# Kernel tuning notes

Measured on AMD Instinct MI355X. Metric: run time of the kernel, lower is better.

The kernel has to match this reference:

```python
import jax, jax.numpy as jnp
import numpy as np
import math

N_STATE = 64
H_MODEL = 1024
D_CONV = 16
EXPAND = 2
D_INNER = EXPAND * H_MODEL            # 2048
HEADDIM = H_MODEL // 4                # 256
NHEADS = D_INNER // HEADDIM           # 8
NGROUPS = 1
CONV_DIM = D_INNER + 2 * NGROUPS * N_STATE           # 2176
D_IN_PROJ = 2 * D_INNER + 2 * NGROUPS * N_STATE + NHEADS
BATCH, SEQLEN = 4, 2048


def setup_inputs() -> dict:
    key = jax.random.key(0)
    ks = jax.random.split(key, 10)
    x = jax.random.normal(ks[0], (BATCH, SEQLEN, H_MODEL), jnp.float32)
    W_in = jax.random.normal(ks[1], (H_MODEL, D_IN_PROJ), jnp.float32) * (H_MODEL ** -0.5)
    conv_w = jax.random.normal(ks[2], (CONV_DIM, D_CONV), jnp.float32) * (D_CONV ** -0.5)
    conv_b = jnp.zeros((CONV_DIM,), jnp.float32)
    # inverse-softplus of dt0 in [1e-3, 1e-1] (mamba2 dt init)
    dt0 = jnp.exp(jax.random.uniform(ks[3], (NHEADS,), minval=math.log(1e-3), maxval=math.log(1e-1)))
    dt_bias = jnp.log(jnp.expm1(dt0))
    A_log = jnp.log(jax.random.uniform(ks[4], (NHEADS,), minval=1.0, maxval=16.0))
    D = jnp.ones((NHEADS,), jnp.float32)
    init_states = jax.random.normal(ks[5], (NHEADS, HEADDIM, N_STATE), jnp.float32) * 0.01
    norm_w = jnp.ones((D_INNER,), jnp.float32)
    W_out = jax.random.normal(ks[6], (D_INNER, H_MODEL), jnp.float32) * (D_INNER ** -0.5)
    W_nl = jax.random.normal(ks[7], (H_MODEL, H_MODEL), jnp.float32) * (H_MODEL ** -0.5)
    b_nl = jnp.zeros((H_MODEL,), jnp.float32)
    return dict(x=x, W_in=W_in, conv_w=conv_w, conv_b=conv_b, dt_bias=dt_bias,
                A_log=A_log, D=D, init_states=init_states, norm_w=norm_w,
                W_out=W_out, W_nl=W_nl, b_nl=b_nl)


def _mamba2(x, W_in, conv_w, conv_b, dt_bias, A_log, D, init_states, norm_w, W_out):
    b, l, _ = x.shape
    zxbcdt = x @ W_in                                  # (b, l, d_in_proj)
    z = zxbcdt[..., :D_INNER]
    xBC = zxbcdt[..., D_INNER:D_INNER + CONV_DIM]
    dt = jax.nn.softplus(zxbcdt[..., -NHEADS:] + dt_bias)   # (b, l, nheads)
    # depthwise causal conv1d (torch conv1d == cross-correlation)
    kernel = conv_w.T[:, None, :]                      # (K, 1, conv_dim)
    xBC = jax.lax.conv_general_dilated(
        xBC, kernel, window_strides=(1,), padding=[(D_CONV - 1, 0)],
        dimension_numbers=('NWC', 'WIO', 'NWC'), feature_group_count=CONV_DIM) + conv_b
    xBC = jax.nn.silu(xBC)
    xs = xBC[..., :D_INNER].reshape(b, l, NHEADS, HEADDIM)  # (b, l, h, p)
    Bm = xBC[..., D_INNER:D_INNER + N_STATE]                 # (b, l, n)
    Cm = xBC[..., D_INNER + N_STATE:]                        # (b, l, n)
    A = -jnp.exp(A_log)                                      # (nheads,) negative
    dA = jnp.exp(dt * A)                                     # (b, l, h)
    h0 = jnp.broadcast_to(init_states, (b, NHEADS, HEADDIM, N_STATE))

    def step(h, inp):
        dA_t, x_t, dt_t, B_t, C_t = inp
        dBx = jnp.einsum('bh,bhp,bn->bhpn', dt_t, x_t, B_t)
        h = h * dA_t[:, :, None, None] + dBx
        y_t = jnp.einsum('bhpn,bn->bhp', h, C_t)
        return h, y_t

    scan_in = (jnp.moveaxis(dA, 1, 0), jnp.moveaxis(xs, 1, 0), jnp.moveaxis(dt, 1, 0),
               jnp.moveaxis(Bm, 1, 0), jnp.moveaxis(Cm, 1, 0))
    _, ys = jax.lax.scan(step, h0, scan_in)
    y = jnp.moveaxis(ys, 0, 1) + D[None, None, :, None] * xs  # D skip connection
    y = y.reshape(b, l, D_INNER)
    # gated RMSNorm: rmsnorm(y * silu(z)) * norm_w, eps=1e-5
    y = y * jax.nn.silu(z)
    y = y * jax.lax.rsqrt(jnp.mean(y * y, axis=-1, keepdims=True) + 1e-5) * norm_w
    return y @ W_out


def reference(x, W_in, conv_w, conv_b, dt_bias, A_log, D, init_states, norm_w, W_out, W_nl, b_nl):
    y = _mamba2(x, W_in, conv_w, conv_b, dt_bias, A_log, D, init_states, norm_w, W_out)
    t = y / jnp.sqrt(1.0 + y * y)   # TanhApprox
    return t @ W_nl + b_nl + x      # Linear + residual
```

## Files before the change

kernel.cpp:

```cpp
#include <hip/hip_runtime.h>
#include <stdint.h>
#include <stddef.h>

#define BATCH   4
#define SEQLEN  2048
#define HM      1024
#define DINNER  2048
#define NH      8
#define HD      256
#define NS      64
#define CONVD   2176
#define DCONV   16
#define DPROJ   4232
#define ROWS    (BATCH*SEQLEN)
#define QC      256
#define NC      (SEQLEN/QC)
#define SC      64
#define TT      16

typedef __attribute__((ext_vector_type(8))) short short8;
typedef __attribute__((ext_vector_type(4))) short short4v;
typedef __attribute__((ext_vector_type(4))) float f32x4;

static constexpr size_t O_WOUT   = 0;
static constexpr size_t O_WNL    = 4194304;
static constexpr size_t O_DT     = 6291456;
static constexpr size_t O_LDA    = 6553600;
static constexpr size_t O_PG     = 6815744;
static constexpr size_t O_BT     = 6819840;
static constexpr size_t O_ZB     = 7868416;
static constexpr size_t O_XBCPRE = 41422848;
static constexpr size_t O_SG     = O_XBCPRE;
static constexpr size_t O_HG     = O_XBCPRE + 16777216;
static constexpr size_t O_TB     = O_XBCPRE;
static constexpr size_t O_XBC    = 77074432;
static constexpr size_t O_YN     = O_XBC;
static constexpr size_t O_XTR    = 112726016;
static constexpr size_t O_XBF    = O_XTR;
static constexpr size_t O_WIN    = O_XTR + 16777216;
static constexpr size_t O_WTAIL  = 146280448;

__device__ __forceinline__ short f2bf(float f) {
  union { float f; uint32_t u; } v; v.f = f;
  uint32_t r = v.u + 0x7fffu + ((v.u >> 16) & 1u);
  return (short)(r >> 16);
}

__device__ __forceinline__ float bf2f(short s) {
  union { float f; uint32_t u; } v;
  v.u = ((uint32_t)(uint16_t)s) << 16;
  return v.f;
}

__device__ __forceinline__ void gload_lds16(const void* g, void* l) {
  __builtin_amdgcn_global_load_lds(
      (const __attribute__((address_space(1))) uint32_t*)g,
      (__attribute__((address_space(3))) uint32_t*)l, 16, 0, 0);
}

__device__ __forceinline__ float sigmoidf_fast(float x) {
  return 1.f / (1.f + __expf(-x));
}

__device__ __forceinline__ short8 fragr(const char* base, int row, int kbyte) {
  return *(const short8*)(base + row * 128 + (kbyte ^ ((row & 7) << 4)));
}

__device__ __forceinline__ void transpose_tile(const float* __restrict__ W,
                                               short* __restrict__ Wt,
                                               int idx, int srcN, int validN,
                                               int Kdim, int nTilesN, int tid) {
  __shared__ short lds[64][72];
  int k0 = (idx / nTilesN) * 64;
  int n0 = (idx % nTilesN) * 64;
  int rr = tid >> 4;
  int cc = (tid & 15) * 4;
#pragma unroll
  for (int pass = 0; pass < 4; ++pass) {
    int k = pass * 16 + rr;
    int gn = n0 + cc;
    f32x4 v = (f32x4)0.f;
    if (gn < validN) v = *(const f32x4*)(W + (size_t)(k0 + k) * srcN + gn);
    uint32_t p0 = (uint32_t)(uint16_t)f2bf(v[0]) | ((uint32_t)(uint16_t)f2bf(v[1]) << 16);
    uint32_t p1 = (uint32_t)(uint16_t)f2bf(v[2]) | ((uint32_t)(uint16_t)f2bf(v[3]) << 16);
    *(uint32_t*)&lds[k][cc] = p0;
    *(uint32_t*)&lds[k][cc + 2] = p1;
  }
  __syncthreads();
  int n = tid >> 2;
  int ks = (tid & 3) * 16;
  short8 a, b;
#pragma unroll
  for (int j = 0; j < 8; ++j) a[j] = lds[ks + j][n];
#pragma unroll
  for (int j = 0; j < 8; ++j) b[j] = lds[ks + 8 + j][n];
  short* dst = Wt + (size_t)(n0 + n) * Kdim + k0 + ks;
  *(short8*)dst = a;
  *(short8*)(dst + 8) = b;
}

__global__ __launch_bounds__(256)
void prep_weights_kernel(const float* __restrict__ W_in, const float* __restrict__ W_out,
                         const float* __restrict__ W_nl,
                         short* __restrict__ winT, short* __restrict__ woutT,
                         short* __restrict__ wnlT, float* __restrict__ wtailT) {
  int bid = blockIdx.x, tid = threadIdx.x;
  if (bid < 1056) {
    transpose_tile(W_in, winT, bid, DPROJ, DPROJ, HM, 66, tid);
  } else if (bid < 1568) {
    transpose_tile(W_out, woutT, bid - 1056, HM, HM, DINNER, 16, tid);
  } else if (bid < 1824) {
    transpose_tile(W_nl, wnlT, bid - 1568, HM, HM, HM, 16, tid);
  } else {
    int i = (bid - 1824) * 256 + tid;
    int h = i >> 10, k = i & 1023;
    wtailT[i] = W_in[(size_t)k * DPROJ + (DPROJ - NH) + h];
  }
}

__global__ __launch_bounds__(256)
void cast_dt_kernel(const float* __restrict__ x, const float* __restrict__ wtailT,
                    const float* __restrict__ dt_bias, const float* __restrict__ A_log,
                    short* __restrict__ xbf, float* __restrict__ dtg,
                    float* __restrict__ ldA) {
  int row = blockIdx.x, tid = threadIdx.x;
  f32x4 xv = ((const f32x4*)(x + (size_t)row * HM))[tid];
  short4v o = { f2bf(xv[0]), f2bf(xv[1]), f2bf(xv[2]), f2bf(xv[3]) };
  ((short4v*)(xbf + (size_t)row * HM))[tid] = o;
  float p[NH];
#pragma unroll
  for (int h = 0; h < NH; ++h) {
    f32x4 w = ((const f32x4*)(wtailT + h * HM))[tid];
    p[h] = xv[0] * w[0] + xv[1] * w[1] + xv[2] * w[2] + xv[3] * w[3];
  }
#pragma unroll
  for (int h = 0; h < NH; ++h)
#pragma unroll
    for (int of = 32; of; of >>= 1) p[h] += __shfl_down(p[h], of);
  __shared__ float red[4][NH];
  int lane = tid & 63, w4 = tid >> 6;
  if (lane == 0)
#pragma unroll
    for (int h = 0; h < NH; ++h) red[w4][h] = p[h];
  __syncthreads();
  if (tid < NH) {
    float s = red[0][tid] + red[1][tid] + red[2][tid] + red[3][tid] + dt_bias[tid];
    float dtv = (s > 20.f) ? s : log1pf(expf(s));
    float A = -expf(A_log[tid]);
    dtg[row * NH + tid] = dtv;
    ldA[row * NH + tid] = dtv * A;
  }
}

__device__ __forceinline__ void prefix_aa(float av, float* aa, float* wsum,
                                          int tid) {
  float v = av;
  int lane = tid & 63;
#pragma unroll
  for (int o = 1; o < 64; o <<= 1) {
    float u = __shfl_up(v, o);
    if (lane >= o) v += u;
  }
  if (lane == 63) wsum[tid >> 6] = v;
  __syncthreads();
  float off = 0.f;
  int w4 = tid >> 6;
#pragma unroll
  for (int w = 0; w < 4; ++w)
    if (w < w4) off += wsum[w];
  aa[tid + 1] = v + off;
  if (tid == 0) aa[0] = 0.f;
  __syncthreads();
}

__global__ __launch_bounds__(512)
void gemm1_256(const short* __restrict__ A, const short* __restrict__ B,
               int K, int nTilesN,
               short* __restrict__ Cb, short* __restrict__ Cb2) {
  __shared__ alignas(16) char lds[49152];
  char* As = lds;
  char* Bs = lds + 32768;
  const int tid = threadIdx.x;
  int bid = blockIdx.x;
  {
    int nwg = gridDim.x;
    if ((nwg & 7) == 0) bid = (bid & 7) * (nwg >> 3) + (bid >> 3);
  }
  const int m0 = (bid / nTilesN) * 256;
  const int n0 = (bid % nTilesN) * 128;
  const int lane = tid & 63;
  const int wid = tid >> 6;
  const int wm = wid >> 1;
  const int wn = wid & 1;
  const int lrow = lane & 15, lk = lane >> 4;

  f32x4 acc[4][4];
#pragma unroll
  for (int i = 0; i < 4; ++i)
#pragma unroll
    for (int j = 0; j < 4; ++j) acc[i][j] = (f32x4)0.f;

  for (int k0 = 0; k0 < K; k0 += 64) {
#pragma unroll
    for (int r = 0; r < 4; ++r) {
      int p = r * 8192 + tid * 16;
      int row = p >> 7, c = p & 127;
      int sc = c ^ ((row & 7) << 4);
      gload_lds16((const char*)A + ((size_t)(m0 + row) * K + k0) * 2 + sc, As + p);
    }
#pragma unroll
    for (int r = 0; r < 2; ++r) {
      int p = r * 8192 + tid * 16;
      int row = p >> 7, c = p & 127;
      int sc = c ^ ((row & 7) << 4);
      gload_lds16((const char*)B + ((size_t)(n0 + row) * K + k0) * 2 + sc, Bs + p);
    }
    asm volatile("s_waitcnt vmcnt(0)" ::: "memory");
    __syncthreads();
#pragma unroll
    for (int ks = 0; ks < 2; ++ks) {
      short8 av[4], bv[4];
#pragma unroll
      for (int i = 0; i < 4; ++i) {
        av[i] = fragr(As, wm * 64 + i * 16 + lrow, ks * 64 + lk * 16);
        bv[i] = fragr(Bs, wn * 64 + i * 16 + lrow, ks * 64 + lk * 16);
      }
#pragma unroll
      for (int i = 0; i < 4; ++i)
#pragma unroll
        for (int j = 0; j < 4; ++j)
          acc[i][j] = __builtin_amdgcn_mfma_f32_16x16x32_bf16(av[i], bv[j], acc[i][j], 0, 0, 0);
    }
    __syncthreads();
  }

  const int row0 = m0 + wm * 64, col0 = n0 + wn * 64;
#pragma unroll
  for (int i = 0; i < 4; ++i)
#pragma unroll
    for (int j = 0; j < 4; ++j)
#pragma unroll
      for (int r = 0; r < 4; ++r) {
        int row = row0 + i * 16 + lk * 4 + r;
        int col = col0 + j * 16 + lrow;
        float v = acc[i][j][r];
        if (col < DINNER) Cb[(size_t)row * DINNER + col] = f2bf(v);
        else if (col < DINNER + CONVD) Cb2[(size_t)row * CONVD + (col - DINNER)] = f2bf(v);
      }
}

template <int EPI>
__global__ __launch_bounds__(512)
void gemm8p(const short* __restrict__ A, const short* __restrict__ B,
            int K, int nTilesN, int N_out,
            float* __restrict__ Cf, short* __restrict__ Cb,
            const float* __restrict__ bias, const float* __restrict__ resid) {
  __shared__ alignas(16) char lds[147456];
  const int tid = threadIdx.x;
  int bid = blockIdx.x;
  {
    int nwg = gridDim.x;
    if ((nwg & 7) == 0) bid = (bid & 7) * (nwg >> 3) + (bid >> 3);
  }
  const int m0 = (bid / nTilesN) * 256;
  const int n0 = (bid % nTilesN) * 128;
  const int lane = tid & 63;
  const int wid = tid >> 6;
  const int wm = wid >> 1;
  const int wn = wid & 1;
  const int lrow = lane & 15, lk = lane >> 4;
  const int nK = K >> 6;

#define LDSA(s) (lds + (s) * 49152)
#define LDSB(s) (lds + (s) * 49152 + 32768)

#define STAGE_A(s, kt, it) do {                                              \
    int p_ = (it) * 8192 + tid * 16;                                         \
    int row_ = p_ >> 7, c_ = p_ & 127;                                       \
    int sc_ = c_ ^ ((row_ & 7) << 4);                                        \
    gload_lds16((const char*)A + ((size_t)(m0 + row_) * K + (kt) * 64) * 2 + sc_, \
                LDSA(s) + p_);                                               \
  } while (0)
#define STAGE_B(s, kt, it) do {                                              \
    int p_ = (it) * 8192 + tid * 16;                                         \
    int row_ = p_ >> 7, c_ = p_ & 127;                                       \
    int sc_ = c_ ^ ((row_ & 7) << 4);                                        \
    gload_lds16((const char*)B + ((size_t)(n0 + row_) * K + (kt) * 64) * 2 + sc_, \
                LDSB(s) + p_);                                               \
  } while (0)

  f32x4 acc[4][4];
#pragma unroll
  for (int i = 0; i < 4; ++i)
#pragma unroll
    for (int j = 0; j < 4; ++j) acc[i][j] = (f32x4)0.f;

#pragma unroll
  for (int it = 0; it < 4; ++it) STAGE_A(0, 0, it);
#pragma unroll
  for (int it = 0; it < 2; ++it) STAGE_B(0, 0, it);
#pragma unroll
  for (int it = 0; it < 4; ++it) STAGE_A(1, 1, it);
#pragma unroll
  for (int it = 0; it < 2; ++it) STAGE_B(1, 1, it);
  asm volatile("s_waitcnt vmcnt(6)" ::: "memory");
  __builtin_amdgcn_s_barrier();

  for (int kt = 0; kt < nK; ++kt) {
    const int rs = kt % 3;
    const int ss = (kt + 2) % 3;
    const bool st = (kt + 2) < nK;
    const char* Ab = LDSA(rs);
    const char* Bb = LDSB(rs);
    short8 aF[4][2], bF[4][2];

#pragma unroll
    for (int ii = 0; ii < 4; ++ii)
#pragma unroll
      for (int ks = 0; ks < 2; ++ks)
        aF[ii][ks] = fragr(Ab, wm * 64 + ii * 16 + lrow, ks * 64 + lk * 16);
#pragma unroll
    for (int jj = 0; jj < 2; ++jj)
#pragma unroll
      for (int ks = 0; ks < 2; ++ks)
        bF[jj][ks] = fragr(Bb, wn * 64 + jj * 16 + lrow, ks * 64 + lk * 16);
    if (st) { STAGE_A(ss, kt + 2, 0); STAGE_A(ss, kt + 2, 1); STAGE_A(ss, kt + 2, 2); STAGE_A(ss, kt + 2, 3); }
    __builtin_amdgcn_s_barrier();
    asm volatile("s_waitcnt lgkmcnt(0)" ::: "memory");
    __builtin_amdgcn_s_setprio(1);
#pragma unroll
    for (int ii = 0; ii < 4; ++ii)
#pragma unroll
      for (int jj = 0; jj < 2; ++jj)
#pragma unroll
        for (int ks = 0; ks < 2; ++ks)
          acc[ii][jj] = __builtin_amdgcn_mfma_f32_16x16x32_bf16(aF[ii][ks], bF[jj][ks], acc[ii][jj], 0, 0, 0);
    __builtin_amdgcn_s_setprio(0);
    __builtin_amdgcn_s_barrier();

#pragma unroll
    for (int jj = 2; jj < 4; ++jj)
#pragma unroll
      for (int ks = 0; ks < 2; ++ks)
        bF[jj][ks] = fragr(Bb, wn * 64 + jj * 16 + lrow, ks * 64 + lk * 16);
    if (st) { STAGE_B(ss, kt + 2, 0); STAGE_B(ss, kt + 2, 1); }
    __builtin_amdgcn_s_barrier();
    asm volatile("s_waitcnt lgkmcnt(0)" ::: "memory");
    __builtin_amdgcn_s_setprio(1);
#pragma unroll
    for (int ii = 0; ii < 4; ++ii)
#pragma unroll
      for (int jj = 2; jj < 4; ++jj)
#pragma unroll
        for (int ks = 0; ks < 2; ++ks)
          acc[ii][jj] = __builtin_amdgcn_mfma_f32_16x16x32_bf16(aF[ii][ks], bF[jj][ks], acc[ii][jj], 0, 0, 0);
    __builtin_amdgcn_s_setprio(0);
    if (kt >= nK - 2) {
      asm volatile("s_waitcnt vmcnt(0)" ::: "memory");
    } else {
      asm volatile("s_waitcnt vmcnt(6)" ::: "memory");
    }
    __builtin_amdgcn_s_barrier();
  }

  const int row0 = m0 + wm * 64, col0 = n0 + wn * 64;
#pragma unroll
  for (int i = 0; i < 4; ++i)
#pragma unroll
    for (int j = 0; j < 4; ++j)
#pragma unroll
      for (int r = 0; r < 4; ++r) {
        int row = row0 + i * 16 + lk * 4 + r;
        int col = col0 + j * 16 + lrow;
        float v = acc[i][j][r];
        if (EPI == 1) {
          float t = v * rsqrtf(1.f + v * v);
          Cb[(size_t)row * N_out + col] = f2bf(t);
        } else if (EPI == 2) {
          Cf[(size_t)row * N_out + col] = v + bias[col] + resid[(size_t)row * N_out + col];
        }
      }
#undef LDSA
#undef LDSB
#undef STAGE_A
#undef STAGE_B
}

__global__ __launch_bounds__(256) void conv_silu_kernel(const short* __restrict__ xbcpre,
                                                        const float* __restrict__ cw,
                                                        const float* __restrict__ cbias,
                                                        short* __restrict__ bc,
                                                        short* __restrict__ xT,
                                                        short* __restrict__ bTg) {
  __shared__ short tld[64][130];
  int blk = blockIdx.x;
  int cg = blk % 17;
  int tg = (blk / 17) % 32;
  int b  = blk / (17 * 32);
  int lane = threadIdx.x & 63;
  int warp = threadIdx.x >> 6;
  int c0 = cg * 128 + lane * 2;
  int tbase = (tg * 4 + warp) * TT;

  const short* inp = xbcpre + (size_t)(b * SEQLEN) * CONVD + c0;
  uint32_t in[TT + DCONV - 1];
#pragma unroll
  for (int j = 0; j < TT + DCONV - 1; ++j) {
    int t = tbase + j - (DCONV - 1);
    in[j] = (t >= 0) ? *(const uint32_t*)(inp + (size_t)t * CONVD) : 0u;
  }
  float w0[DCONV], w1[DCONV];
  const float* wp = cw + (size_t)c0 * DCONV;
#pragma unroll
  for (int k = 0; k < DCONV; ++k) { w0[k] = wp[k]; w1[k] = wp[DCONV + k]; }
  float bb0 = cbias[c0], bb1 = cbias[c0 + 1];

  const bool isBC = (cg == 16);
  short* bcp = bc + (size_t)(b * SEQLEN) * 128 + (c0 - DINNER);
#pragma unroll
  for (int tt = 0; tt < TT; ++tt) {
    float a0 = bb0, a1 = bb1;
#pragma unroll
    for (int k = 0; k < DCONV; ++k) {
      uint32_t v = in[tt + k];
      a0 = fmaf(bf2f((short)(v & 0xffffu)), w0[k], a0);
      a1 = fmaf(bf2f((short)(v >> 16)), w1[k], a1);
    }
    a0 = a0 * sigmoidf_fast(a0);
    a1 = a1 * sigmoidf_fast(a1);
    uint32_t o = (uint32_t)(uint16_t)f2bf(a0) | ((uint32_t)(uint16_t)f2bf(a1) << 16);
    if (isBC) *(uint32_t*)(bcp + (size_t)(tbase + tt) * 128) = o;
    *(uint32_t*)&tld[warp * TT + tt][lane * 2] = o;
  }
  __syncthreads();
  int ch = threadIdx.x & 127;
  int seg = threadIdx.x >> 7;
  int gc = cg * 128 + ch;
  short* dst = nullptr;
  if (gc < DINNER) dst = xT + (size_t)gc * ROWS;
  else if (gc < DINNER + NS) dst = bTg + (size_t)(gc - DINNER) * ROWS;
  if (dst) {
    int tcol = b * SEQLEN + tg * 64 + seg * 32;
    short8 v[4];
#pragma unroll
    for (int q = 0; q < 4; ++q)
#pragma unroll
      for (int j = 0; j < 8; ++j) v[q][j] = tld[seg * 32 + q * 8 + j][ch];
    short8* dp = (short8*)(dst + tcol);
    dp[0] = v[0]; dp[1] = v[1]; dp[2] = v[2]; dp[3] = v[3];
  }
}

__global__ __launch_bounds__(256)
void scan_passA_mfma(const short* __restrict__ xT, const short* __restrict__ bTg,
                     const float* __restrict__ dtg, const float* __restrict__ ldA,
                     float* __restrict__ Sg, float* __restrict__ Pg) {
  __shared__ alignas(16) char Ax[16384];
  __shared__ alignas(16) char Bt[8192];
  __shared__ float aa[QC + 1];
  __shared__ float wdt[QC];
  __shared__ float wsum[4];
  int blk2 = blockIdx.x;
  int half = blk2 & 1, blk = blk2 >> 1;
  int c8 = blk & 7, bh = blk >> 3;
  int h = bh & 7, b = bh >> 3;
  int pbase = half * 128;
  int tid = threadIdx.x, wave = tid >> 6, lane = tid & 63;
  int lrow = lane & 15, lk = lane >> 4;
  int rowbase = b * SEQLEN + c8 * QC;
  prefix_aa(ldA[(rowbase + tid) * NH + h], aa, wsum, tid);
  float alast = aa[QC];
  if (tid == 0 && half == 0) Pg[blk] = __expf(alast);
  wdt[tid] = __expf(alast - aa[tid + 1]) * dtg[(rowbase + tid) * NH + h];

  f32x4 acc[2][4];
#pragma unroll
  for (int i = 0; i < 2; ++i)
#pragma unroll
    for (int j = 0; j < 4; ++j) acc[i][j] = (f32x4)0.f;

  for (int ks = 0; ks < 4; ++ks) {
    int s0 = ks * 64;
#pragma unroll
    for (int it = 0; it < 4; ++it) {
      int p = it * 4096 + tid * 16;
      int row = p >> 7, c = p & 127;
      int sc = c ^ ((row & 7) << 4);
      gload_lds16((const char*)(xT + (size_t)(h * HD + pbase + row) * ROWS + rowbase + s0) + sc, Ax + p);
    }
#pragma unroll
    for (int it = 0; it < 2; ++it) {
      int p = it * 4096 + tid * 16;
      int row = p >> 7, c = p & 127;
      int sc = c ^ ((row & 7) << 4);
      gload_lds16((const char*)(bTg + (size_t)row * ROWS + rowbase + s0) + sc, Bt + p);
    }
    asm volatile("s_waitcnt vmcnt(0)" ::: "memory");
    __syncthreads();
    {
      int row = wave * 32 + (lane & 31);
      int gb = (lane >> 5) * 4;
#pragma unroll
      for (int gi = 0; gi < 4; ++gi) {
        int g = gb + gi;
        int off = row * 128 + g * 16;
        int sb = s0 + (((g * 16) ^ ((row & 7) << 4)) >> 1);
        short8 v = *(short8*)(Ax + off);
        short8 o;
#pragma unroll
        for (int j = 0; j < 8; ++j) o[j] = f2bf(bf2f(v[j]) * wdt[sb + j]);
        *(short8*)(Ax + off) = o;
      }
    }
    __syncthreads();
#pragma unroll
    for (int kk = 0; kk < 2; ++kk) {
      short8 av[2], bv[4];
#pragma unroll
      for (int i = 0; i < 2; ++i)
        av[i] = fragr(Ax, wave * 32 + i * 16 + lrow, kk * 64 + lk * 16);
#pragma unroll
      for (int j = 0; j < 4; ++j)
        bv[j] = fragr(Bt, j * 16 + lrow, kk * 64 + lk * 16);
#pragma unroll
      for (int i = 0; i < 2; ++i)
#pragma unroll
        for (int j = 0; j < 4; ++j)
          acc[i][j] = __builtin_amdgcn_mfma_f32_16x16x32_bf16(av[i], bv[j], acc[i][j], 0, 0, 0);
    }
    __syncthreads();
  }
#pragma unroll
  for (int i = 0; i < 2; ++i)
#pragma unroll
    for (int j = 0; j < 4; ++j)
#pragma unroll
      for (int r = 0; r < 4; ++r) {
        int p = pbase + wave * 32 + i * 16 + lk * 4 + r;
        int n = j * 16 + lrow;
        Sg[((size_t)blk * 256 + p) * 64 + n] = acc[i][j][r];
      }
}

__global__ __launch_bounds__(256)
void scan_passB(const float* __restrict__ Sg, const float* __restrict__ Pg,
                const float* __restrict__ init, float* __restrict__ Hg) {
  int blk = blockIdx.x;
  int ptile = blk & 15, bh = blk >> 4;
  int h = bh & (NH - 1);
  int tid = threadIdx.x;
  size_t off = (size_t)ptile * 1024 + tid * 4;
  f32x4 hc = *(const f32x4*)(init + (size_t)h * HD * NS + off);
#pragma unroll 1
  for (int c = 0; c < NC; ++c) {
    *(f32x4*)(Hg + (size_t)(bh * NC + c) * 16384 + off) = hc;
    float P = Pg[bh * NC + c];
    f32x4 s = *(const f32x4*)(Sg + (size_t)(bh * NC + c) * 16384 + off);
    hc = P * hc + s;
  }
}

__global__ __launch_bounds__(256)
void scan_passC_mfma(const short* __restrict__ xT, const short* __restrict__ bTg,
                     const short* __restrict__ bc,
                     const float* __restrict__ dtg, const float* __restrict__ ldA,
                     const float* __restrict__ Hg, const float* __restrict__ Dp,
                     short* __restrict__ yfull) {
  __shared__ alignas(16) char Xb[16384];
  __shared__ alignas(16) char Hb[16384];
  __shared__ alignas(16) char Bn[8192];
  __shared__ alignas(16) char Cn[8192];
  __shared__ alignas(16) char Bt2[8192];
  __shared__ alignas(16) char Mm[8192];
  __shared__ float aa[QC + 1];
  __shared__ float dts[QC];
  __shared__ float wsum[4];
  int blk2 = blockIdx.x;
  int half = blk2 & 1, blk = blk2 >> 1;
  int c8 = blk & 7, bh = blk >> 3;
  int h = bh & 7, b = bh >> 3;
  int pbase = half * 128;
  int tid = threadIdx.x, wave = tid >> 6, lane = tid & 63;
  int lrow = lane & 15, lk = lane >> 4;
  int rowbase = b * SEQLEN + c8 * QC;
  prefix_aa(ldA[(rowbase + tid) * NH + h], aa, wsum, tid);
  dts[tid] = dtg[(rowbase + tid) * NH + h];
  __syncthreads();
  float Dh = Dp[h];

  f32x4 hcc[2][4];
  const float* hp = Hg + (size_t)blk * 16384;
#pragma unroll
  for (int i = 0; i < 2; ++i)
#pragma unroll
    for (int j = 0; j < 4; ++j)
#pragma unroll
      for (int r = 0; r < 4; ++r)
        hcc[i][j][r] = hp[(size_t)(pbase + wave * 32 + i * 16 + lk * 4 + r) * 64 + j * 16 + lrow];

  for (int sc = 0; sc < 4; ++sc) {
    int s0 = sc * SC;
#pragma unroll
    for (int i = 0; i < 2; ++i)
#pragma unroll
      for (int j = 0; j < 4; ++j)
#pragma unroll
        for (int r = 0; r < 4; ++r) {
          int pl = wave * 32 + i * 16 + lk * 4 + r;
          int n = j * 16 + lrow;
          *(short*)(Hb + pl * 128 + ((n * 2) ^ ((pl & 7) << 4))) = f2bf(hcc[i][j][r]);
        }
#pragma unroll
    for (int it = 0; it < 4; ++it) {
      int p = it * 4096 + tid * 16;
      int row = p >> 7, c = p & 127;
      int scz = c ^ ((row & 7) << 4);
      gload_lds16((const char*)(xT + (size_t)(h * HD + pbase + row) * ROWS + rowbase + s0) + scz, Xb + p);
    }
#pragma unroll
    for (int it = 0; it < 2; ++it) {
      int p = it * 4096 + tid * 16;
      int row = p >> 7, c = p & 127;
      int scz = c ^ ((row & 7) << 4);
      gload_lds16((const char*)(bc + (size_t)(rowbase + s0 + row) * 128) + scz, Bn + p);
      gload_lds16((const char*)(bc + (size_t)(rowbase + s0 + row) * 128 + NS) + scz, Cn + p);
      gload_lds16((const char*)(bTg + (size_t)row * ROWS + rowbase + s0) + scz, Bt2 + p);
    }
    asm volatile("s_waitcnt vmcnt(0)" ::: "memory");
    __syncthreads();

    f32x4 gcc[4];
#pragma unroll
    for (int j = 0; j < 4; ++j) gcc[j] = (f32x4)0.f;
#pragma unroll
    for (int kk = 0; kk < 2; ++kk) {
      short8 avc = fragr(Cn, wave * 16 + lrow, kk * 64 + lk * 16);
#pragma unroll
      for (int j = 0; j < 4; ++j) {
        short8 bvb = fragr(Bn, j * 16 + lrow, kk * 64 + lk * 16);
        gcc[j] = __builtin_amdgcn_mfma_f32_16x16x32_bf16(avc, bvb, gcc[j], 0, 0, 0);
      }
    }
#pragma unroll
    for (int j = 0; j < 4; ++j)
#pragma unroll
      for (int r = 0; r < 4; ++r) {
        int t = wave * 16 + lk * 4 + r;
        int s = j * 16 + lrow;
        float val = (s <= t) ? gcc[j][r] * __expf(aa[s0 + t + 1] - aa[s0 + s + 1]) * dts[s0 + s]
                             : 0.f;
        *(short*)(Mm + t * 128 + ((s * 2) ^ ((t & 7) << 4))) = f2bf(val);
      }
#pragma unroll
    for (int pass = 0; pass < 2; ++pass) {
      int t = wave * 16 + (lane >> 3) + pass * 8;
      int g = lane & 7;
      int off = t * 128 + g * 16;
      float fac = __expf(aa[s0 + t + 1] - aa[s0]);
      short8 v = *(short8*)(Cn + off);
      short8 o;
#pragma unroll
      for (int j = 0; j < 8; ++j) o[j] = f2bf(bf2f(v[j]) * fac);
      *(short8*)(Cn + off) = o;
    }
    __syncthreads();

    f32x4 ycc[4][2];
#pragma unroll
    for (int i = 0; i < 4; ++i)
#pragma unroll
      for (int j = 0; j < 2; ++j) ycc[i][j] = (f32x4)0.f;
#pragma unroll
    for (int kk = 0; kk < 2; ++kk) {
      short8 av[4], bv[2];
#pragma unroll
      for (int i = 0; i < 4; ++i)
        av[i] = fragr(Mm, i * 16 + lrow, kk * 64 + lk * 16);
#pragma unroll
      for (int j = 0; j < 2; ++j)
        bv[j] = fragr(Xb, wave * 32 + j * 16 + lrow, kk * 64 + lk * 16);
#pragma unroll
      for (int i = 0; i < 4; ++i)
#pragma unroll
        for (int j = 0; j < 2; ++j)
          ycc[i][j] = __builtin_amdgcn_mfma_f32_16x16x32_bf16(av[i], bv[j], ycc[i][j], 0, 0, 0);
    }
#pragma unroll
    for (int kk = 0; kk < 2; ++kk) {
      short8 av[4], bv[2];
#pragma unroll
      for (int i = 0; i < 4; ++i)
        av[i] = fragr(Cn, i * 16 + lrow, kk * 64 + lk * 16);
#pragma unroll
      for (int j = 0; j < 2; ++j)
        bv[j] = fragr(Hb, wave * 32 + j * 16 + lrow, kk * 64 + lk * 16);
#pragma unroll
      for (int i = 0; i < 4; ++i)
#pragma unroll
        for (int j = 0; j < 2; ++j)
          ycc[i][j] = __builtin_amdgcn_mfma_f32_16x16x32_bf16(av[i], bv[j], ycc[i][j], 0, 0, 0);
    }
#pragma unroll
    for (int i = 0; i < 4; ++i)
#pragma unroll
      for (int j = 0; j < 2; ++j)
#pragma unroll
        for (int r = 0; r < 4; ++r) {
          int t = i * 16 + lk * 4 + r;
          int pl = wave * 32 + j * 16 + lrow;
          float xv = bf2f(*(const short*)(Xb + pl * 128 + ((t * 2) ^ ((pl & 7) << 4))));
          yfull[(size_t)(rowbase + s0 + t) * DINNER + h * HD + pbase + pl] = f2bf(ycc[i][j][r] + Dh * xv);
        }
    {
      int row = wave * 32 + (lane & 31);
      int gb = (lane >> 5) * 4;
      float aend = aa[s0 + SC];
#pragma unroll
      for (int gi = 0; gi < 4; ++gi) {
        int g = gb + gi;
        int off = row * 128 + g * 16;
        int sb = s0 + (((g * 16) ^ ((row & 7) << 4)) >> 1);
        short8 v = *(short8*)(Xb + off);
        short8 o;
#pragma unroll
        for (int j = 0; j < 8; ++j)
          o[j] = f2bf(bf2f(v[j]) * __expf(aend - aa[sb + j + 1]) * dts[sb + j]);
        *(short8*)(Xb + off) = o;
      }
    }
    {
      float Ps = __expf(aa[s0 + SC] - aa[s0]);
#pragma unroll
      for (int i = 0; i < 2; ++i)
#pragma unroll
        for (int j = 0; j < 4; ++j) hcc[i][j] *= Ps;
#pragma unroll
      for (int kk = 0; kk < 2; ++kk) {
        short8 av[2], bv[4];
#pragma unroll
        for (int i = 0; i < 2; ++i)
          av[i] = fragr(Xb, wave * 32 + i * 16 + lrow, kk * 64 + lk * 16);
#pragma unroll
        for (int j = 0; j < 4; ++j)
          bv[j] = fragr(Bt2, j * 16 + lrow, kk * 64 + lk * 16);
#pragma unroll
        for (int i = 0; i < 2; ++i)
#pragma unroll
          for (int j = 0; j < 4; ++j)
            hcc[i][j] = __builtin_amdgcn_mfma_f32_16x16x32_bf16(av[i], bv[j], hcc[i][j], 0, 0, 0);
      }
    }
    __syncthreads();
  }
}

__global__ __launch_bounds__(256)
void gate_norm_kernel(const short* __restrict__ yfull, const short* __restrict__ zb,
                      const float* __restrict__ norm_w, short* __restrict__ yn) {
  int row = blockIdx.x, tid = threadIdx.x;
  size_t yb = (size_t)row * DINNER;
  float v[8];
  float ss = 0.f;
#pragma unroll
  for (int g = 0; g < 2; ++g) {
    int cidx = g * 1024 + tid * 4;
    short4v y4 = *(const short4v*)(yfull + yb + cidx);
    short4v z4 = *(const short4v*)(zb + yb + cidx);
#pragma unroll
    for (int j = 0; j < 4; ++j) {
      float z = bf2f(z4[j]);
      float val = bf2f(y4[j]) * z * sigmoidf_fast(z);
      v[g * 4 + j] = val;
      ss = fmaf(val, val, ss);
    }
  }
#pragma unroll
  for (int o = 32; o; o >>= 1) ss += __shfl_down(ss, o);
  __shared__ float red[4];
  if ((tid & 63) == 0) red[tid >> 6] = ss;
  __syncthreads();
  float tot = red[0] + red[1] + red[2] + red[3];
  float scale = rsqrtf(tot * (1.f / (float)DINNER) + 1e-5f);
#pragma unroll
  for (int g = 0; g < 2; ++g) {
    int cidx = g * 1024 + tid * 4;
    short4v o4;
#pragma unroll
    for (int j = 0; j < 4; ++j) o4[j] = f2bf(v[g * 4 + j] * scale * norm_w[cidx + j]);
    *(short4v*)(yn + yb + cidx) = o4;
  }
}

extern "C" void kernel_launch(void* const* d_in, const int* in_sizes, int n_in,
                              void* d_out, int out_size, void* d_ws, size_t ws_size,
                              hipStream_t stream) {
  (void)in_sizes; (void)n_in; (void)out_size; (void)ws_size;
  const float* x     = (const float*)d_in[0];
  const float* W_in  = (const float*)d_in[1];
  const float* convw = (const float*)d_in[2];
  const float* convb = (const float*)d_in[3];
  const float* dtb   = (const float*)d_in[4];
  const float* Alog  = (const float*)d_in[5];
  const float* Dp    = (const float*)d_in[6];
  const float* inis  = (const float*)d_in[7];
  const float* nw    = (const float*)d_in[8];
  const float* W_out = (const float*)d_in[9];
  const float* W_nl  = (const float*)d_in[10];
  const float* b_nl  = (const float*)d_in[11];
  float* out = (float*)d_out;
  char* ws = (char*)d_ws;

  short* woutT  = (short*)(ws + O_WOUT);
  short* wnlT   = (short*)(ws + O_WNL);
  float* dtg    = (float*)(ws + O_DT);
  float* ldA    = (float*)(ws + O_LDA);
  float* Pg     = (float*)(ws + O_PG);
  short* bTg    = (short*)(ws + O_BT);
  short* zb     = (short*)(ws + O_ZB);
  short* xbcpre = (short*)(ws + O_XBCPRE);
  float* Sg     = (float*)(ws + O_SG);
  float* Hg     = (float*)(ws + O_HG);
  short* tb     = (short*)(ws + O_TB);
  short* bc     = (short*)(ws + O_XBC);
  short* yn     = (short*)(ws + O_YN);
  short* xT     = (short*)(ws + O_XTR);
  short* xbf    = (short*)(ws + O_XBF);
  short* winT   = (short*)(ws + O_WIN);
  float* wtailT = (float*)(ws + O_WTAIL);
  short* yfull  = (short*)d_out;

  prep_weights_kernel<<<1856, 256, 0, stream>>>(W_in, W_out, W_nl, winT, woutT, wnlT, wtailT);
  cast_dt_kernel<<<ROWS, 256, 0, stream>>>(x, wtailT, dtb, Alog, xbf, dtg, ldA);

  gemm1_256<<<32 * 33, 512, 0, stream>>>(xbf, winT, HM, 33, zb, xbcpre);
  conv_silu_kernel<<<17 * 32 * 4, 256, 0, stream>>>(xbcpre, convw, convb, bc, xT, bTg);

  scan_passA_mfma<<<32 * NC * 2, 256, 0, stream>>>(xT, bTg, dtg, ldA, Sg, Pg);
  scan_passB<<<32 * 16, 256, 0, stream>>>(Sg, Pg, inis, Hg);
  scan_passC_mfma<<<32 * NC * 2, 256, 0, stream>>>(xT, bTg, bc, dtg, ldA, Hg, Dp, yfull);

  gate_norm_kernel<<<ROWS, 256, 0, stream>>>(yfull, zb, nw, yn);
  gemm8p<1><<<32 * 8, 512, 0, stream>>>(yn, woutT, DINNER, 8, HM, nullptr, tb, nullptr, nullptr);
  gemm8p<2><<<32 * 8, 512, 0, stream>>>(tb, wnlT, HM, 8, HM, out, nullptr, b_nl, x);
}
```

Measured before the change: 289.9 us.

## Fuse gated RMSNorm into scan output and out-projection epilogue

The gate multiply (y*silu(z)) and the per-row sum of squares move into the scan pass-C epilogue, which writes partial sums per row. A tiny kernel reduces these into per-row inverse RMS, which the W_out GEMM epilogue then applies; norm_w is folded into the transposed W_out weights during prep. This removes the separate gate_norm pass, which read and wrote a full activation tensor. It also adds XCD-aware block remapping to the scan passes. In exchange, pass C now reads z with strided scalar loads and does extra shuffles, and the normalisation is applied after the bf16 matmul rather than before it.

Result: slower. 304.2 us (+5.0%).

```diff
diff --git a/kernel.cpp b/kernel.cpp
--- a/kernel.cpp
+++ b/kernel.cpp
@@ -34,11 +34,12 @@
 static constexpr size_t O_HG     = O_XBCPRE + 16777216;
 static constexpr size_t O_TB     = O_XBCPRE;
 static constexpr size_t O_XBC    = 77074432;
-static constexpr size_t O_YN     = O_XBC;
 static constexpr size_t O_XTR    = 112726016;
 static constexpr size_t O_XBF    = O_XTR;
 static constexpr size_t O_WIN    = O_XTR + 16777216;
 static constexpr size_t O_WTAIL  = 146280448;
+static constexpr size_t O_PSUM   = 146313216;
+static constexpr size_t O_INVR   = 148410368;
 
 __device__ __forceinline__ short f2bf(float f) {
   union { float f; uint32_t u; } v; v.f = f;
@@ -69,7 +70,8 @@
 __device__ __forceinline__ void transpose_tile(const float* __restrict__ W,
                                                short* __restrict__ Wt,
                                                int idx, int srcN, int validN,
-                                               int Kdim, int nTilesN, int tid) {
+                                               int Kdim, int nTilesN, int tid,
+                                               const float* __restrict__ kscale) {
   __shared__ short lds[64][72];
   int k0 = (idx / nTilesN) * 64;
   int n0 = (idx % nTilesN) * 64;
@@ -81,6 +83,10 @@
     int gn = n0 + cc;
     f32x4 v = (f32x4)0.f;
     if (gn < validN) v = *(const f32x4*)(W + (size_t)(k0 + k) * srcN + gn);
+    if (kscale) {
+      float s = kscale[k0 + k];
+      v[0] *= s; v[1] *= s; v[2] *= s; v[3] *= s;
+    }
     uint32_t p0 = (uint32_t)(uint16_t)f2bf(v[0]) | ((uint32_t)(uint16_t)f2bf(v[1]) << 16);
     uint32_t p1 = (uint32_t)(uint16_t)f2bf(v[2]) | ((uint32_t)(uint16_t)f2bf(v[3]) << 16);
     *(uint32_t*)&lds[k][cc] = p0;
@@ -101,16 +107,16 @@
 
 __global__ __launch_bounds__(256)
 void prep_weights_kernel(const float* __restrict__ W_in, const float* __restrict__ W_out,
-                         const float* __restrict__ W_nl,
+                         const float* __restrict__ W_nl, const float* __restrict__ nw,
                          short* __restrict__ winT, short* __restrict__ woutT,
                          short* __restrict__ wnlT, float* __restrict__ wtailT) {
   int bid = blockIdx.x, tid = threadIdx.x;
   if (bid < 1056) {
-    transpose_tile(W_in, winT, bid, DPROJ, DPROJ, HM, 66, tid);
+    transpose_tile(W_in, winT, bid, DPROJ, DPROJ, HM, 66, tid, nullptr);
   } else if (bid < 1568) {
-    transpose_tile(W_out, woutT, bid - 1056, HM, HM, DINNER, 16, tid);
+    transpose_tile(W_out, woutT, bid - 1056, HM, HM, DINNER, 16, tid, nw);
   } else if (bid < 1824) {
-    transpose_tile(W_nl, wnlT, bid - 1568, HM, HM, HM, 16, tid);
+    transpose_tile(W_nl, wnlT, bid - 1568, HM, HM, HM, 16, tid, nullptr);
   } else {
     int i = (bid - 1824) * 256 + tid;
     int h = i >> 10, k = i & 1023;
@@ -254,7 +260,8 @@
 void gemm8p(const short* __restrict__ A, const short* __restrict__ B,
             int K, int nTilesN, int N_out,
             float* __restrict__ Cf, short* __restrict__ Cb,
-            const float* __restrict__ bias, const float* __restrict__ resid) {
+            const float* __restrict__ bias, const float* __restrict__ resid,
+            const float* __restrict__ invr) {
   __shared__ alignas(16) char lds[147456];
   const int tid = threadIdx.x;
   int bid = blockIdx.x;
@@ -374,7 +381,8 @@
         int col = col0 + j * 16 + lrow;
         float v = acc[i][j][r];
         if (EPI == 1) {
-          float t = v * rsqrtf(1.f + v * v);
+          float vv = v * invr[row];
+          float t = vv * rsqrtf(1.f + vv * vv);
           Cb[(size_t)row * N_out + col] = f2bf(t);
         } else if (EPI == 2) {
           Cf[(size_t)row * N_out + col] = v + bias[col] + resid[(size_t)row * N_out + col];
@@ -461,6 +469,10 @@
   __shared__ float wdt[QC];
   __shared__ float wsum[4];
   int blk2 = blockIdx.x;
+  {
+    int nwg = gridDim.x;
+    if ((nwg & 7) == 0) blk2 = (blk2 & 7) * (nwg >> 3) + (blk2 >> 3);
+  }
   int half = blk2 & 1, blk = blk2 >> 1;
   int c8 = blk & 7, bh = blk >> 3;
   int h = bh & 7, b = bh >> 3;
@@ -562,10 +574,10 @@
 
 __global__ __launch_bounds__(256)
 void scan_passC_mfma(const short* __restrict__ xT, const short* __restrict__ bTg,
-                     const short* __restrict__ bc,
+                     const short* __restrict__ bc, const short* __restrict__ zb,
                      const float* __restrict__ dtg, const float* __restrict__ ldA,
                      const float* __restrict__ Hg, const float* __restrict__ Dp,
-                     short* __restrict__ yfull) {
+                     float* __restrict__ psum, short* __restrict__ yfull) {
   __shared__ alignas(16) char Xb[16384];
   __shared__ alignas(16) char Hb[16384];
   __shared__ alignas(16) char Bn[8192];
@@ -576,6 +588,10 @@
   __shared__ float dts[QC];
   __shared__ float wsum[4];
   int blk2 = blockIdx.x;
+  {
+    int nwg = gridDim.x;
+    if ((nwg & 7) == 0) blk2 = (blk2 & 7) * (nwg >> 3) + (blk2 >> 3);
+  }
   int half = blk2 & 1, blk = blk2 >> 1;
   int c8 = blk & 7, bh = blk >> 3;
   int h = bh & 7, b = bh >> 3;
@@ -587,6 +603,7 @@
   dts[tid] = dtg[(rowbase + tid) * NH + h];
   __syncthreads();
   float Dh = Dp[h];
+  const int slot = (h * 2 + half) * 4 + wave;
 
   f32x4 hcc[2][4];
   const float* hp = Hg + (size_t)blk * 16384;
@@ -703,14 +720,24 @@
 #pragma unroll
     for (int i = 0; i < 4; ++i)
 #pragma unroll
-      for (int j = 0; j < 2; ++j)
-#pragma unroll
-        for (int r = 0; r < 4; ++r) {
-          int t = i * 16 + lk * 4 + r;
+      for (int r = 0; r < 4; ++r) {
+        int t = i * 16 + lk * 4 + r;
+        size_t grow = (size_t)(rowbase + s0 + t);
+        float pq = 0.f;
+#pragma unroll
+        for (int j = 0; j < 2; ++j) {
           int pl = wave * 32 + j * 16 + lrow;
           float xv = bf2f(*(const short*)(Xb + pl * 128 + ((t * 2) ^ ((pl & 7) << 4))));
-          yfull[(size_t)(rowbase + s0 + t) * DINNER + h * HD + pbase + pl] = f2bf(ycc[i][j][r] + Dh * xv);
+          float yv = ycc[i][j][r] + Dh * xv;
+          float zv = bf2f(zb[grow * DINNER + h * HD + pbase + pl]);
+          float val = yv * zv * sigmoidf_fast(zv);
+          yfull[grow * DINNER + h * HD + pbase + pl] = f2bf(val);
+          pq = fmaf(val, val, pq);
         }
+#pragma unroll
+        for (int m = 1; m < 16; m <<= 1) pq += __shfl_xor(pq, m);
+        if (lrow == 0) psum[grow * 64 + slot] = pq;
+      }
     {
       int row = wave * 32 + (lane & 31);
       int gb = (lane >> 5) * 4;
@@ -755,40 +782,13 @@
 }
 
 __global__ __launch_bounds__(256)
-void gate_norm_kernel(const short* __restrict__ yfull, const short* __restrict__ zb,
-                      const float* __restrict__ norm_w, short* __restrict__ yn) {
-  int row = blockIdx.x, tid = threadIdx.x;
-  size_t yb = (size_t)row * DINNER;
-  float v[8];
-  float ss = 0.f;
-#pragma unroll
-  for (int g = 0; g < 2; ++g) {
-    int cidx = g * 1024 + tid * 4;
-    short4v y4 = *(const short4v*)(yfull + yb + cidx);
-    short4v z4 = *(const short4v*)(zb + yb + cidx);
-#pragma unroll
-    for (int j = 0; j < 4; ++j) {
-      float z = bf2f(z4[j]);
-      float val = bf2f(y4[j]) * z * sigmoidf_fast(z);
-      v[g * 4 + j] = val;
-      ss = fmaf(val, val, ss);
-    }
-  }
-#pragma unroll
-  for (int o = 32; o; o >>= 1) ss += __shfl_down(ss, o);
-  __shared__ float red[4];
-  if ((tid & 63) == 0) red[tid >> 6] = ss;
-  __syncthreads();
-  float tot = red[0] + red[1] + red[2] + red[3];
-  float scale = rsqrtf(tot * (1.f / (float)DINNER) + 1e-5f);
-#pragma unroll
-  for (int g = 0; g < 2; ++g) {
-    int cidx = g * 1024 + tid * 4;
-    short4v o4;
-#pragma unroll
-    for (int j = 0; j < 4; ++j) o4[j] = f2bf(v[g * 4 + j] * scale * norm_w[cidx + j]);
-    *(short4v*)(yn + yb + cidx) = o4;
-  }
+void invrms_kernel(const float* __restrict__ psum, float* __restrict__ invr) {
+  int row = blockIdx.x * 256 + threadIdx.x;
+  const f32x4* p = (const f32x4*)(psum + (size_t)row * 64);
+  float s = 0.f;
+#pragma unroll
+  for (int q = 0; q < 16; ++q) { f32x4 v = p[q]; s += (v[0] + v[1]) + (v[2] + v[3]); }
+  invr[row] = rsqrtf(s * (1.f / (float)DINNER) + 1e-5f);
 }
 
 extern "C" void kernel_launch(void* const* d_in, const int* in_sizes, int n_in,
@@ -822,14 +822,15 @@
   float* Hg     = (float*)(ws + O_HG);
   short* tb     = (short*)(ws + O_TB);
   short* bc     = (short*)(ws + O_XBC);
-  short* yn     = (short*)(ws + O_YN);
   short* xT     = (short*)(ws + O_XTR);
   short* xbf    = (short*)(ws + O_XBF);
   short* winT   = (short*)(ws + O_WIN);
   float* wtailT = (float*)(ws + O_WTAIL);
+  float* psum   = (float*)(ws + O_PSUM);
+  float* invr   = (float*)(ws + O_INVR);
   short* yfull  = (short*)d_out;
 
-  prep_weights_kernel<<<1856, 256, 0, stream>>>(W_in, W_out, W_nl, winT, woutT, wnlT, wtailT);
+  prep_weights_kernel<<<1856, 256, 0, stream>>>(W_in, W_out, W_nl, nw, winT, woutT, wnlT, wtailT);
   cast_dt_kernel<<<ROWS, 256, 0, stream>>>(x, wtailT, dtb, Alog, xbf, dtg, ldA);
 
   gemm1_256<<<32 * 33, 512, 0, stream>>>(xbf, winT, HM, 33, zb, xbcpre);
@@ -837,9 +838,9 @@
 
   scan_passA_mfma<<<32 * NC * 2, 256, 0, stream>>>(xT, bTg, dtg, ldA, Sg, Pg);
   scan_passB<<<32 * 16, 256, 0, stream>>>(Sg, Pg, inis, Hg);
-  scan_passC_mfma<<<32 * NC * 2, 256, 0, stream>>>(xT, bTg, bc, dtg, ldA, Hg, Dp, yfull);
-
-  gate_norm_kernel<<<ROWS, 256, 0, stream>>>(yfull, zb, nw, yn);
-  gemm8p<1><<<32 * 8, 512, 0, stream>>>(yn, woutT, DINNER, 8, HM, nullptr, tb, nullptr, nullptr);
-  gemm8p<2><<<32 * 8, 512, 0, stream>>>(tb, wnlT, HM, 8, HM, out, nullptr, b_nl, x);
-}
+  scan_passC_mfma<<<32 * NC * 2, 256, 0, stream>>>(xT, bTg, bc, zb, dtg, ldA, Hg, Dp, psum, yfull);
+
+  invrms_kernel<<<32, 256, 0, stream>>>(psum, invr);
+  gemm8p<1><<<32 * 8, 512, 0, stream>>>(yfull, woutT, DINNER, 8, HM, nullptr, tb, nullptr, nullptr, invr);
+  gemm8p<2><<<32 * 8, 512, 0, stream>>>(tb, wnlT, HM, 8, HM, out, nullptr, b_nl, x, nullptr);
+}
```

## Store scan chunk states in bf16 and merge weight prep with cast kernel

Applied to the files above, without the earlier changes.

Chunk-state partial sums (Sg) and the propagated inter-chunk states (Hg) are now stored as bf16 instead of fp32. This halves the memory traffic of passA's writes, passB's reads and writes, and passC's state loads. The weight-transpose work and the x-cast/dt computation are fused into one launch, with a tiny separate kernel producing the dt weight tail first. Storing states in bf16 loses precision in the recurrent state accumulation inputs, which may raise numerical error.

Measured after the change: 287.1 us. Within noise of the previous version (-1.0%).

```diff
diff --git a/kernel.cpp b/kernel.cpp
--- a/kernel.cpp
+++ b/kernel.cpp
@@ -31,7 +31,7 @@
 static constexpr size_t O_ZB     = 7868416;
 static constexpr size_t O_XBCPRE = 41422848;
 static constexpr size_t O_SG     = O_XBCPRE;
-static constexpr size_t O_HG     = O_XBCPRE + 16777216;
+static constexpr size_t O_HG     = O_XBCPRE + 8388608;
 static constexpr size_t O_TB     = O_XBCPRE;
 static constexpr size_t O_XBC    = 77074432;
 static constexpr size_t O_YN     = O_XBC;
@@ -64,6 +64,13 @@
 
 __device__ __forceinline__ short8 fragr(const char* base, int row, int kbyte) {
   return *(const short8*)(base + row * 128 + (kbyte ^ ((row & 7) << 4)));
+}
+
+__global__ __launch_bounds__(256)
+void wtail_kernel(const float* __restrict__ W_in, float* __restrict__ wtailT) {
+  int i = blockIdx.x * 256 + threadIdx.x;
+  int h = i >> 10, k = i & 1023;
+  wtailT[i] = W_in[(size_t)k * DPROJ + (DPROJ - NH) + h];
 }
 
 __device__ __forceinline__ void transpose_tile(const float* __restrict__ W,
@@ -100,10 +107,14 @@
 }
 
 __global__ __launch_bounds__(256)
-void prep_weights_kernel(const float* __restrict__ W_in, const float* __restrict__ W_out,
-                         const float* __restrict__ W_nl,
-                         short* __restrict__ winT, short* __restrict__ woutT,
-                         short* __restrict__ wnlT, float* __restrict__ wtailT) {
+void prep_cast_kernel(const float* __restrict__ W_in, const float* __restrict__ W_out,
+                      const float* __restrict__ W_nl,
+                      short* __restrict__ winT, short* __restrict__ woutT,
+                      short* __restrict__ wnlT,
+                      const float* __restrict__ x, const float* __restrict__ wtailT,
+                      const float* __restrict__ dt_bias, const float* __restrict__ A_log,
+                      short* __restrict__ xbf, float* __restrict__ dtg,
+                      float* __restrict__ ldA) {
   int bid = blockIdx.x, tid = threadIdx.x;
   if (bid < 1056) {
     transpose_tile(W_in, winT, bid, DPROJ, DPROJ, HM, 66, tid);
@@ -112,43 +123,33 @@
   } else if (bid < 1824) {
     transpose_tile(W_nl, wnlT, bid - 1568, HM, HM, HM, 16, tid);
   } else {
-    int i = (bid - 1824) * 256 + tid;
-    int h = i >> 10, k = i & 1023;
-    wtailT[i] = W_in[(size_t)k * DPROJ + (DPROJ - NH) + h];
-  }
-}
-
-__global__ __launch_bounds__(256)
-void cast_dt_kernel(const float* __restrict__ x, const float* __restrict__ wtailT,
-                    const float* __restrict__ dt_bias, const float* __restrict__ A_log,
-                    short* __restrict__ xbf, float* __restrict__ dtg,
-                    float* __restrict__ ldA) {
-  int row = blockIdx.x, tid = threadIdx.x;
-  f32x4 xv = ((const f32x4*)(x + (size_t)row * HM))[tid];
-  short4v o = { f2bf(xv[0]), f2bf(xv[1]), f2bf(xv[2]), f2bf(xv[3]) };
-  ((short4v*)(xbf + (size_t)row * HM))[tid] = o;
-  float p[NH];
-#pragma unroll
-  for (int h = 0; h < NH; ++h) {
-    f32x4 w = ((const f32x4*)(wtailT + h * HM))[tid];
-    p[h] = xv[0] * w[0] + xv[1] * w[1] + xv[2] * w[2] + xv[3] * w[3];
-  }
-#pragma unroll
-  for (int h = 0; h < NH; ++h)
-#pragma unroll
-    for (int of = 32; of; of >>= 1) p[h] += __shfl_down(p[h], of);
-  __shared__ float red[4][NH];
-  int lane = tid & 63, w4 = tid >> 6;
-  if (lane == 0)
-#pragma unroll
-    for (int h = 0; h < NH; ++h) red[w4][h] = p[h];
-  __syncthreads();
-  if (tid < NH) {
-    float s = red[0][tid] + red[1][tid] + red[2][tid] + red[3][tid] + dt_bias[tid];
-    float dtv = (s > 20.f) ? s : log1pf(expf(s));
-    float A = -expf(A_log[tid]);
-    dtg[row * NH + tid] = dtv;
-    ldA[row * NH + tid] = dtv * A;
+    int row = bid - 1824;
+    f32x4 xv = ((const f32x4*)(x + (size_t)row * HM))[tid];
+    short4v o = { f2bf(xv[0]), f2bf(xv[1]), f2bf(xv[2]), f2bf(xv[3]) };
+    ((short4v*)(xbf + (size_t)row * HM))[tid] = o;
+    float p[NH];
+#pragma unroll
+    for (int h = 0; h < NH; ++h) {
+      f32x4 w = ((const f32x4*)(wtailT + h * HM))[tid];
+      p[h] = xv[0] * w[0] + xv[1] * w[1] + xv[2] * w[2] + xv[3] * w[3];
+    }
+#pragma unroll
+    for (int h = 0; h < NH; ++h)
+#pragma unroll
+      for (int of = 32; of; of >>= 1) p[h] += __shfl_down(p[h], of);
+    __shared__ float red[4][NH];
+    int lane = tid & 63, w4 = tid >> 6;
+    if (lane == 0)
+#pragma unroll
+      for (int h = 0; h < NH; ++h) red[w4][h] = p[h];
+    __syncthreads();
+    if (tid < NH) {
+      float s = red[0][tid] + red[1][tid] + red[2][tid] + red[3][tid] + dt_bias[tid];
+      float dtv = (s > 20.f) ? s : log1pf(expf(s));
+      float A = -expf(A_log[tid]);
+      dtg[row * NH + tid] = dtv;
+      ldA[row * NH + tid] = dtv * A;
+    }
   }
 }
 
@@ -454,7 +455,7 @@
 __global__ __launch_bounds__(256)
 void scan_passA_mfma(const short* __restrict__ xT, const short* __restrict__ bTg,
                      const float* __restrict__ dtg, const float* __restrict__ ldA,
-                     float* __restrict__ Sg, float* __restrict__ Pg) {
+                     short* __restrict__ Sg, float* __restrict__ Pg) {
   __shared__ alignas(16) char Ax[16384];
   __shared__ alignas(16) char Bt[8192];
   __shared__ float aa[QC + 1];
@@ -538,13 +539,13 @@
       for (int r = 0; r < 4; ++r) {
         int p = pbase + wave * 32 + i * 16 + lk * 4 + r;
         int n = j * 16 + lrow;
-        Sg[((size_t)blk * 256 + p) * 64 + n] = acc[i][j][r];
+        Sg[((size_t)blk * 256 + p) * 64 + n] = f2bf(acc[i][j][r]);
       }
 }
 
 __global__ __launch_bounds__(256)
-void scan_passB(const float* __restrict__ Sg, const float* __restrict__ Pg,
-                const float* __restrict__ init, float* __restrict__ Hg) {
+void scan_passB(const short* __restrict__ Sg, const float* __restrict__ Pg,
+                const float* __restrict__ init, short* __restrict__ Hg) {
   int blk = blockIdx.x;
   int ptile = blk & 15, bh = blk >> 4;
   int h = bh & (NH - 1);
@@ -553,10 +554,14 @@
   f32x4 hc = *(const f32x4*)(init + (size_t)h * HD * NS + off);
 #pragma unroll 1
   for (int c = 0; c < NC; ++c) {
-    *(f32x4*)(Hg + (size_t)(bh * NC + c) * 16384 + off) = hc;
+    short4v hb = { f2bf(hc[0]), f2bf(hc[1]), f2bf(hc[2]), f2bf(hc[3]) };
+    *(short4v*)(Hg + (size_t)(bh * NC + c) * 16384 + off) = hb;
     float P = Pg[bh * NC + c];
-    f32x4 s = *(const f32x4*)(Sg + (size_t)(bh * NC + c) * 16384 + off);
-    hc = P * hc + s;
+    short4v s4 = *(const short4v*)(Sg + (size_t)(bh * NC + c) * 16384 + off);
+    hc[0] = P * hc[0] + bf2f(s4[0]);
+    hc[1] = P * hc[1] + bf2f(s4[1]);
+    hc[2] = P * hc[2] + bf2f(s4[2]);
+    hc[3] = P * hc[3] + bf2f(s4[3]);
   }
 }
 
@@ -564,7 +569,7 @@
 void scan_passC_mfma(const short* __restrict__ xT, const short* __restrict__ bTg,
                      const short* __restrict__ bc,
                      const float* __restrict__ dtg, const float* __restrict__ ldA,
-                     const float* __restrict__ Hg, const float* __restrict__ Dp,
+                     const short* __restrict__ Hg, const float* __restrict__ Dp,
                      short* __restrict__ yfull) {
   __shared__ alignas(16) char Xb[16384];
   __shared__ alignas(16) char Hb[16384];
@@ -589,14 +594,14 @@
   float Dh = Dp[h];
 
   f32x4 hcc[2][4];
-  const float* hp = Hg + (size_t)blk * 16384;
+  const short* hp = Hg + (size_t)blk * 16384;
 #pragma unroll
   for (int i = 0; i < 2; ++i)
 #pragma unroll
     for (int j = 0; j < 4; ++j)
 #pragma unroll
       for (int r = 0; r < 4; ++r)
-        hcc[i][j][r] = hp[(size_t)(pbase + wave * 32 + i * 16 + lk * 4 + r) * 64 + j * 16 + lrow];
+        hcc[i][j][r] = bf2f(hp[(size_t)(pbase + wave * 32 + i * 16 + lk * 4 + r) * 64 + j * 16 + lrow]);
 
   for (int sc = 0; sc < 4; ++sc) {
     int s0 = sc * SC;
@@ -818,8 +823,8 @@
   short* bTg    = (short*)(ws + O_BT);
   short* zb     = (short*)(ws + O_ZB);
   short* xbcpre = (short*)(ws + O_XBCPRE);
-  float* Sg     = (float*)(ws + O_SG);
-  float* Hg     = (float*)(ws + O_HG);
+  short* Sg     = (short*)(ws + O_SG);
+  short* Hg     = (short*)(ws + O_HG);
   short* tb     = (short*)(ws + O_TB);
   short* bc     = (short*)(ws + O_XBC);
   short* yn     = (short*)(ws + O_YN);
@@ -829,8 +834,9 @@
   float* wtailT = (float*)(ws + O_WTAIL);
   short* yfull  = (short*)d_out;
 
-  prep_weights_kernel<<<1856, 256, 0, stream>>>(W_in, W_out, W_nl, winT, woutT, wnlT, wtailT);
-  cast_dt_kernel<<<ROWS, 256, 0, stream>>>(x, wtailT, dtb, Alog, xbf, dtg, ldA);
+  wtail_kernel<<<32, 256, 0, stream>>>(W_in, wtailT);
+  prep_cast_kernel<<<1824 + ROWS, 256, 0, stream>>>(W_in, W_out, W_nl, winT, woutT, wnlT,
+                                                    x, wtailT, dtb, Alog, xbf, dtg, ldA);
 
   gemm1_256<<<32 * 33, 512, 0, stream>>>(xbf, winT, HM, 33, zb, xbcpre);
   conv_silu_kernel<<<17 * 32 * 4, 256, 0, stream>>>(xbcpre, convw, convb, bc, xT, bTg);
```
